# Optimization experiments

Hardware: AMD Instinct MI355X
Metric: run time of the kernel (lower is better)

The kernel has to match this reference:

```python
import jax, jax.numpy as jnp
import numpy as np
from jax import lax

EPS = 1e-5

def _sign(x):
    # sign with sign(0)=+1, as used in XNOR-style binarization
    return jnp.where(x >= 0, 1.0, -1.0).astype(x.dtype)

def binarize(x):
    # straight-through estimator: forward = sign(x), backward = identity
    return x + lax.stop_gradient(_sign(x) - x)

def batchnorm(x, p):
    # p: [4, C] rows = (gamma, beta, running_mean, running_var); eval-mode BN
    g, b, m, v = p[0], p[1], p[2], p[3]
    shape = (1, -1) + (1,) * (x.ndim - 2)
    inv = g / jnp.sqrt(v + EPS)
    return (x - m.reshape(shape)) * inv.reshape(shape) + b.reshape(shape)

def conv2d(x, w):
    return lax.conv_general_dilated(x, w, window_strides=(1, 1), padding='VALID',
                                    dimension_numbers=('NCHW', 'OIHW', 'NCHW'))

def maxpool2(x):
    return lax.reduce_window(x, -jnp.inf, lax.max, (1, 1, 2, 2), (1, 1, 2, 2), 'VALID')

def hardtanh(x):
    return jnp.clip(x, -1.0, 1.0)


def setup_inputs() -> dict:
    key = jax.random.key(0)
    ks = jax.random.split(key, 16)
    B = 16384
    x = jax.random.normal(ks[0], (B, 3, 22, 22), jnp.float32)
    w1 = jax.random.normal(ks[1], (32, 3, 3, 3), jnp.float32) * 0.1
    w2 = jax.random.normal(ks[2], (32, 32, 3, 3), jnp.float32) * 0.1
    w3 = jax.random.normal(ks[3], (64, 32, 3, 3), jnp.float32) * 0.1
    w_fc1 = jax.random.normal(ks[4], (128, 64), jnp.float32) * 0.1
    w_fc2 = jax.random.normal(ks[5], (2, 128), jnp.float32) * 0.1
    w_fc3 = jax.random.normal(ks[6], (4, 128), jnp.float32) * 0.1

    def make_bn(k, c):
        k1, k2, k3, k4 = jax.random.split(k, 4)
        gamma = jax.random.uniform(k1, (c,), jnp.float32, 0.5, 1.5)
        beta = jax.random.normal(k2, (c,), jnp.float32) * 0.1
        mean = jax.random.normal(k3, (c,), jnp.float32) * 0.1
        var = jax.random.uniform(k4, (c,), jnp.float32, 0.5, 1.5)
        return jnp.stack([gamma, beta, mean, var])  # [4, C]

    bn1 = make_bn(ks[7], 32)
    bn2 = make_bn(ks[8], 32)
    bn3 = make_bn(ks[9], 64)
    bn4 = make_bn(ks[10], 128)
    bn5 = make_bn(ks[11], 2)
    bn6 = make_bn(ks[12], 4)
    return {'x': x, 'w1': w1, 'w2': w2, 'w3': w3, 'w_fc1': w_fc1, 'w_fc2': w_fc2,
            'w_fc3': w_fc3, 'bn1': bn1, 'bn2': bn2, 'bn3': bn3, 'bn4': bn4,
            'bn5': bn5, 'bn6': bn6}


def reference(x, w1, w2, w3, w_fc1, w_fc2, w_fc3, bn1, bn2, bn3, bn4, bn5, bn6):
    # binary=True, binarize_input=True, bitwidth=input_bitwidth=1:
    # every BinarizeConv2d/BinarizeLinear binarizes both its input and weights.
    h = hardtanh(batchnorm(conv2d(binarize(x), binarize(w1)), bn1))   # [B,32,20,20]
    h = maxpool2(h)                                                    # [B,32,10,10]
    h = hardtanh(batchnorm(conv2d(binarize(h), binarize(w2)), bn2))   # [B,32,8,8]
    h = maxpool2(h)                                                    # [B,32,4,4]
    h = hardtanh(batchnorm(conv2d(binarize(h), binarize(w3)), bn3))   # [B,64,2,2]
    h = maxpool2(h)                                                    # [B,64,1,1]
    h = h.reshape(-1, 64)                                              # [B,64]
    h = hardtanh(batchnorm(binarize(h) @ binarize(w_fc1).T, bn4))      # [B,128]
    out1 = jax.nn.softmax(batchnorm(h @ w_fc2.T, bn5), axis=1)         # [B,2]
    out2 = batchnorm(h @ w_fc3.T, bn6)                                 # [B,4]
    return (out1, out2)
```

## Files before the change

### kernel.cpp

```cpp
#include <hip/hip_runtime.h>
#include <cstdint>
#include <cmath>

typedef int  v4i  __attribute__((ext_vector_type(4)));
typedef int  v16i __attribute__((ext_vector_type(16)));
typedef unsigned int u32x4 __attribute__((ext_vector_type(4)));

#define OFF_W1   0
#define OFF_T1   32
#define OFF_W3   384
#define OFF_T3   960
#define OFF_WFC1 1024
#define OFF_A4   1280
#define OFF_C4   1408
#define OFF_WF2  1536
#define OFF_WF3  1792
#define OFF_BN5  2304
#define OFF_BN6  2308
#define OFF_B2   2560
#define OFF_T2C  4864

__device__ __forceinline__ int thr_neg(double nterms, double g, double b, double m, double v) {
    double inv = g / sqrt(v + 1e-5);
    double t = m - b / inv;
    double thr = floor((nterms - t) * 0.5);
    if (thr < -2147000000.0) thr = -2147000000.0;
    if (thr >  2147000000.0) thr =  2147000000.0;
    return -((int)thr + 1);
}

__device__ __forceinline__ int thr_c_neg(double g, double b, double m, double v) {
    double inv = g / sqrt(v + 1e-5);
    double t = m - b / inv;
    double ct = ceil(t);
    if (ct < -2147000000.0) ct = -2147000000.0;
    if (ct >  2147000000.0) ct =  2147000000.0;
    return -(int)ct;
}

__global__ void k_prep(const float* __restrict__ w1, const float* __restrict__ w2,
                       const float* __restrict__ w3, const float* __restrict__ wfc1,
                       const float* __restrict__ wfc2, const float* __restrict__ wfc3,
                       const float* __restrict__ bn1, const float* __restrict__ bn2,
                       const float* __restrict__ bn3, const float* __restrict__ bn4,
                       const float* __restrict__ bn5, const float* __restrict__ bn6,
                       unsigned int* __restrict__ ws) {
    __shared__ float stage[9216];
    int t = threadIdx.x;
    int blk = blockIdx.x;
    float* wsf = (float*)ws;
    int*   wsi = (int*)ws;

    if (blk == 0) {
        for (int i = t; i < 864; i += 256) stage[i] = w1[i];
        __syncthreads();
        if (t < 32) {
            unsigned int bits = 0;
            for (int j = 0; j < 27; ++j) bits |= (stage[t*27+j] >= 0.f ? 1u : 0u) << j;
            ws[OFF_W1 + t] = bits;
            wsi[OFF_T1 + t]  = thr_neg(27.0, bn1[t], bn1[32+t], bn1[64+t], bn1[96+t]);
            wsi[OFF_T2C + t] = thr_c_neg(bn2[t], bn2[32+t], bn2[64+t], bn2[96+t]);
        }
        for (int i = t; i < 256; i += 256) wsf[OFF_WF2 + i] = wfc2[i];
        for (int i = t; i < 512; i += 256) wsf[OFF_WF3 + i] = wfc3[i];
        if (t < 2) {
            float g = bn5[t], b = bn5[2+t], m = bn5[4+t], v = bn5[6+t];
            float inv = g / sqrtf(v + 1e-5f);
            wsf[OFF_BN5 + t]     = inv;
            wsf[OFF_BN5 + 2 + t] = b - m * inv;
        }
        if (t >= 4 && t < 8) {
            int j = t - 4;
            float g = bn6[j], b = bn6[4+j], m = bn6[8+j], v = bn6[12+j];
            float inv = g / sqrtf(v + 1e-5f);
            wsf[OFF_BN6 + j]     = inv;
            wsf[OFF_BN6 + 4 + j] = b - m * inv;
        }
    } else if (blk == 1) {
        for (int i = t; i < 9216; i += 256) stage[i] = w2[i];
        __syncthreads();
        for (int idx = t; idx < 2304; idx += 256) {
            int s   = idx >> 8;
            int rem = idx & 255;
            int l   = rem >> 2;
            int reg = rem & 3;
            int och = l & 31;
            int icb = ((l >> 5) << 4) + (reg << 2);
            unsigned int wv = 0;
            #pragma unroll
            for (int j = 0; j < 4; ++j) {
                int ic = icb + j;
                unsigned int by = (stage[(och*32 + ic)*9 + s] >= 0.f) ? 0x01u : 0xFFu;
                wv |= by << (8*j);
            }
            ws[OFF_B2 + idx] = wv;
        }
    } else if (blk == 2 || blk == 3) {
        int base = (blk - 2) * 9216;
        for (int i = t; i < 9216; i += 256) stage[i] = w3[base + i];
        __syncthreads();
        for (int idx = t; idx < 288; idx += 256) {
            int o = idx / 9, k = idx - o*9;
            unsigned int bits = 0;
            for (int i = 0; i < 32; ++i)
                bits |= (stage[(o*32+i)*9 + k] >= 0.f ? 1u : 0u) << i;
            ws[OFF_W3 + base/32 + idx] = bits;
        }
    } else {
        for (int i = t; i < 8192; i += 256) stage[i] = wfc1[i];
        __syncthreads();
        if (t < 128) {
            unsigned int lo = 0, hi = 0;
            for (int j = 0; j < 32; ++j) lo |= (stage[t*64+j]    >= 0.f ? 1u : 0u) << j;
            for (int j = 0; j < 32; ++j) hi |= (stage[t*64+32+j] >= 0.f ? 1u : 0u) << j;
            ws[OFF_WFC1 + 2*t]     = lo;
            ws[OFF_WFC1 + 2*t + 1] = hi;
            float g = bn4[t], b = bn4[128+t], m = bn4[256+t], v = bn4[384+t];
            float inv = g / sqrtf(v + 1e-5f);
            wsf[OFF_A4 + t] = -2.f * inv;
            wsf[OFF_C4 + t] = (64.f - m) * inv + b;
        }
        if (t >= 128 && t < 192) {
            int j = t - 128;
            wsi[OFF_T3 + j] = thr_neg(288.0, bn3[j], bn3[64+j], bn3[128+j], bn3[192+j]);
        }
    }
}

#define WSTRIDE 900
__global__ __launch_bounds__(512, 6) void k_main(const float* __restrict__ x,
                                                 const unsigned int* __restrict__ ws,
                                                 float* __restrict__ out, int B) {
    __shared__ __align__(16) unsigned int s_u[8 * WSTRIDE + 2304];

    const int tid = threadIdx.x & 63;
    const int wid = threadIdx.x >> 6;
    const float* wsf = (const float*)ws;
    const int*   wsi = (const int*)ws;

    unsigned int* Blds  = s_u + 8 * WSTRIDE;
    unsigned int* bytes = s_u + wid * WSTRIDE;
    unsigned int* inrow = bytes;
    unsigned int* c1    = bytes + 66;
    unsigned int* pb1   = bytes + 800;

    for (int i = threadIdx.x; i < 576; i += 512)
        *(u32x4*)(Blds + i*4) = *(const u32x4*)(ws + OFF_B2 + i*4);
    __syncthreads();

    const int b = blockIdx.x * 8 + wid;
    if (b >= B) return;

    const int nthr2 = wsi[OFF_T2C + (tid & 31)];

    for (int r = tid; r < 66; r += 64) {
        int c = r / 22, y = r - c*22;
        const float2* p = (const float2*)(x + ((size_t)b*3 + c)*484 + (size_t)y*22);
        unsigned int w = 0;
        #pragma unroll
        for (int j = 10; j >= 0; --j) {
            float2 v = p[j];
            w = __builtin_amdgcn_alignbit(w, __float_as_uint(v.y), 31);
            w = __builtin_amdgcn_alignbit(w, __float_as_uint(v.x), 31);
        }
        inrow[r] = ~w;
    }
    __builtin_amdgcn_wave_barrier();

    for (int pos = tid; pos < 400; pos += 64) {
        int y = pos / 20, xx = pos - y*20;
        unsigned int g = 0;
        #pragma unroll
        for (int c = 0; c < 3; ++c)
            #pragma unroll
            for (int dy = 0; dy < 3; ++dy)
                g |= ((inrow[c*22 + y + dy] >> xx) & 7u) << (c*9 + dy*3);
        unsigned int word = 0;
        #pragma unroll
        for (int o = 31; o >= 0; --o) {
            unsigned int s = (unsigned int)(__popc(g ^ ws[OFF_W1 + o]) + wsi[OFF_T1 + o]);
            word = __builtin_amdgcn_alignbit(word, s, 31);
        }
        c1[pos] = word;
    }
    __builtin_amdgcn_wave_barrier();

    for (int p = tid; p < 100; p += 64) {
        int py = p / 10, px = p - py*10;
        int base = (2*py)*20 + 2*px;
        pb1[p] = c1[base] | c1[base+1] | c1[base+20] | c1[base+21];
    }
    __builtin_amdgcn_wave_barrier();

    #pragma unroll
    for (int i = 0; i < 4; ++i) {
        int c2 = tid + 64*i;
        if (c2 < 200) {
            int hi  = (c2 >= 100) ? 1 : 0;
            int pos = c2 - hi*100;
            unsigned int w = pb1[pos];
            int sh = hi << 4;
            u32x4 o;
            #pragma unroll
            for (int j = 0; j < 4; ++j) {
                unsigned int nib = (w >> (sh + 4*j)) & 0xFu;
                unsigned int sp  = (nib * 0x204081u) & 0x01010101u;
                o[j] = __builtin_amdgcn_perm(0u, 0x000001FFu, sp);
            }
            *(u32x4*)(bytes + c2*4) = o;
        }
    }
    __builtin_amdgcn_wave_barrier();

    unsigned int pb2w[16];
    {
        const int hi = tid >> 5;
        const int r  = tid & 31;
        #pragma unroll
        for (int tile = 0; tile < 2; ++tile) {
            int gq  = tile*8 + (r >> 2);
            int sub = r & 3;
            int y   = ((gq >> 2) << 1) + (sub >> 1);
            int x   = ((gq & 3) << 1) + (sub & 1);
            const v4i* __restrict__ Ab = (const v4i*)(bytes + (hi*100 + y*10 + x)*4);
            const v4i* __restrict__ Bb = (const v4i*)(Blds + tid*4);
            v16i acc;
            #pragma unroll
            for (int j = 0; j < 16; ++j) acc[j] = nthr2;
            __builtin_amdgcn_s_setprio(1);
            #pragma unroll
            for (int s = 0; s < 9; ++s) {
                int dy = s / 3, dx = s - dy*3;
                v4i a  = Ab[dy*10 + dx];
                v4i bf = Bb[s*64];
                acc = __builtin_amdgcn_mfma_i32_32x32x32_i8(a, bf, acc, 0, 0, 0);
            }
            __builtin_amdgcn_s_setprio(0);
            #pragma unroll
            for (int g = 0; g < 4; ++g) {
                int m0 = acc[4*g]   > acc[4*g+1] ? acc[4*g]   : acc[4*g+1];
                int m1 = acc[4*g+2] > acc[4*g+3] ? acc[4*g+2] : acc[4*g+3];
                int mx = m0 > m1 ? m0 : m1;
                unsigned long long bal = __ballot(mx >= 0);
                pb2w[tile*8 + 2*g]     = (unsigned int)bal;
                pb2w[tile*8 + 2*g + 1] = (unsigned int)(bal >> 32);
            }
        }
    }

    unsigned int w3r[9];
    #pragma unroll
    for (int k = 0; k < 9; ++k) w3r[k] = ws[OFF_W3 + tid*9 + k];
    const int negt3 = wsi[OFF_T3 + tid];

    unsigned long long b3 = 0;
    {
        unsigned int oracc = 0;
        #pragma unroll
        for (int py = 0; py < 2; ++py)
            #pragma unroll
            for (int px = 0; px < 2; ++px) {
                int s = negt3;
                #pragma unroll
                for (int dy = 0; dy < 3; ++dy)
                    #pragma unroll
                    for (int dx = 0; dx < 3; ++dx)
                        s += __popc(pb2w[(py+dy)*4 + px + dx] ^ w3r[dy*3+dx]);
                oracc |= (unsigned int)s;
            }
        b3 = __ballot((int)oracc < 0);
    }

    float h0, h1;
    {
        const unsigned long long* wfc1b = (const unsigned long long*)(ws + OFF_WFC1);
        int pc0 = __popcll(b3 ^ wfc1b[tid]);
        int pc1 = __popcll(b3 ^ wfc1b[tid + 64]);
        float p0 = fmaf((float)pc0, wsf[OFF_A4 + tid],      wsf[OFF_C4 + tid]);
        float p1 = fmaf((float)pc1, wsf[OFF_A4 + tid + 64], wsf[OFF_C4 + tid + 64]);
        h0 = fminf(1.f, fmaxf(-1.f, p0));
        h1 = fminf(1.f, fmaxf(-1.f, p1));
    }

    {
        float part[6];
        #pragma unroll
        for (int j = 0; j < 2; ++j)
            part[j] = h0 * wsf[OFF_WF2 + j*128 + tid] + h1 * wsf[OFF_WF2 + j*128 + 64 + tid];
        #pragma unroll
        for (int j = 0; j < 4; ++j)
            part[2+j] = h0 * wsf[OFF_WF3 + j*128 + tid] + h1 * wsf[OFF_WF3 + j*128 + 64 + tid];
        #pragma unroll
        for (int off = 32; off; off >>= 1) {
            #pragma unroll
            for (int j = 0; j < 6; ++j)
                part[j] += __shfl_xor(part[j], off);
        }
        if (tid < 6) {
            if (tid < 2) {
                float y0 = part[0]*wsf[OFF_BN5+0] + wsf[OFF_BN5+2];
                float y1 = part[1]*wsf[OFF_BN5+1] + wsf[OFF_BN5+3];
                float mx = fmaxf(y0, y1);
                float e0 = expf(y0 - mx), e1 = expf(y1 - mx);
                float r  = 1.f / (e0 + e1);
                out[(size_t)b*2 + tid] = (tid == 0 ? e0 : e1) * r;
            } else {
                int j = tid - 2;
                out[(size_t)B*2 + (size_t)b*4 + j] = part[2+j]*wsf[OFF_BN6+j] + wsf[OFF_BN6+4+j];
            }
        }
    }
}

extern "C" void kernel_launch(void* const* d_in, const int* in_sizes, int n_in,
                              void* d_out, int out_size, void* d_ws, size_t ws_size,
                              hipStream_t stream) {
    const float* x    = (const float*)d_in[0];
    const float* w1   = (const float*)d_in[1];
    const float* w2   = (const float*)d_in[2];
    const float* w3   = (const float*)d_in[3];
    const float* wfc1 = (const float*)d_in[4];
    const float* wfc2 = (const float*)d_in[5];
    const float* wfc3 = (const float*)d_in[6];
    const float* bn1  = (const float*)d_in[7];
    const float* bn2  = (const float*)d_in[8];
    const float* bn3  = (const float*)d_in[9];
    const float* bn4  = (const float*)d_in[10];
    const float* bn5  = (const float*)d_in[11];
    const float* bn6  = (const float*)d_in[12];
    unsigned int* ws  = (unsigned int*)d_ws;
    float* out        = (float*)d_out;
    int B = in_sizes[0] / 1452;

    k_prep<<<5, 256, 0, stream>>>(w1, w2, w3, wfc1, wfc2, wfc3,
                                  bn1, bn2, bn3, bn4, bn5, bn6, ws);
    k_main<<<(B + 7) / 8, 512, 0, stream>>>(x, ws, out, B);
}
```

Before: 182.4 us.

## Fuse conv1, maxpool and byte expansion per pooled output position

Each thread now computes the four conv1 outputs of a 2x2 pool window directly from the input bit rows. It takes the min of the four sign-test sums and writes the expanded byte operand for conv2, so the c1 and pb1 LDS buffers and two wave barriers are gone. This removes the LDS round trips and shrinks per-wave shared memory, which may help occupancy. It loads each weight and threshold once and reuses it across four popcounts. The cost is more registers and fewer active lanes, since 100 pooled positions now spread over 64 threads instead of 400 conv outputs.

```diff
diff --git a/kernel.cpp b/kernel.cpp
--- a/kernel.cpp
+++ b/kernel.cpp
@@ -127,7 +127,7 @@
     }
 }
 
-#define WSTRIDE 900
+#define WSTRIDE 868
 __global__ __launch_bounds__(512, 6) void k_main(const float* __restrict__ x,
                                                  const unsigned int* __restrict__ ws,
                                                  float* __restrict__ out, int B) {
@@ -139,10 +139,8 @@
     const int*   wsi = (const int*)ws;
 
     unsigned int* Blds  = s_u + 8 * WSTRIDE;
-    unsigned int* bytes = s_u + wid * WSTRIDE;
-    unsigned int* inrow = bytes;
-    unsigned int* c1    = bytes + 66;
-    unsigned int* pb1   = bytes + 800;
+    unsigned int* inrow = s_u + wid * WSTRIDE;
+    unsigned int* bytes = inrow + 68;
 
     for (int i = threadIdx.x; i < 576; i += 512)
         *(u32x4*)(Blds + i*4) = *(const u32x4*)(ws + OFF_B2 + i*4);
@@ -167,47 +165,56 @@
     }
     __builtin_amdgcn_wave_barrier();
 
-    for (int pos = tid; pos < 400; pos += 64) {
-        int y = pos / 20, xx = pos - y*20;
-        unsigned int g = 0;
-        #pragma unroll
-        for (int c = 0; c < 3; ++c)
-            #pragma unroll
-            for (int dy = 0; dy < 3; ++dy)
-                g |= ((inrow[c*22 + y + dy] >> xx) & 7u) << (c*9 + dy*3);
-        unsigned int word = 0;
-        #pragma unroll
-        for (int o = 31; o >= 0; --o) {
-            unsigned int s = (unsigned int)(__popc(g ^ ws[OFF_W1 + o]) + wsi[OFF_T1 + o]);
-            word = __builtin_amdgcn_alignbit(word, s, 31);
-        }
-        c1[pos] = word;
-    }
-    __builtin_amdgcn_wave_barrier();
-
-    for (int p = tid; p < 100; p += 64) {
-        int py = p / 10, px = p - py*10;
-        int base = (2*py)*20 + 2*px;
-        pb1[p] = c1[base] | c1[base+1] | c1[base+20] | c1[base+21];
-    }
-    __builtin_amdgcn_wave_barrier();
-
     #pragma unroll
-    for (int i = 0; i < 4; ++i) {
-        int c2 = tid + 64*i;
-        if (c2 < 200) {
-            int hi  = (c2 >= 100) ? 1 : 0;
-            int pos = c2 - hi*100;
-            unsigned int w = pb1[pos];
-            int sh = hi << 4;
-            u32x4 o;
-            #pragma unroll
-            for (int j = 0; j < 4; ++j) {
-                unsigned int nib = (w >> (sh + 4*j)) & 0xFu;
-                unsigned int sp  = (nib * 0x204081u) & 0x01010101u;
-                o[j] = __builtin_amdgcn_perm(0u, 0x000001FFu, sp);
-            }
-            *(u32x4*)(bytes + c2*4) = o;
+    for (int it = 0; it < 2; ++it) {
+        int q = tid + 64*it;
+        if (q < 100) {
+            int py = q / 10, px = q - py*10;
+            unsigned int g00 = 0, g01 = 0, g10 = 0, g11 = 0;
+            #pragma unroll
+            for (int c = 0; c < 3; ++c) {
+                unsigned int a0, a1, a2, a3, b0, b1, b2, b3;
+                {
+                    unsigned int w0 = (inrow[c*22 + 2*py + 0] >> (2*px)) & 15u;
+                    unsigned int w1 = (inrow[c*22 + 2*py + 1] >> (2*px)) & 15u;
+                    unsigned int w2 = (inrow[c*22 + 2*py + 2] >> (2*px)) & 15u;
+                    unsigned int w3 = (inrow[c*22 + 2*py + 3] >> (2*px)) & 15u;
+                    a0 = w0 & 7u; b0 = (w0 >> 1) & 7u;
+                    a1 = w1 & 7u; b1 = (w1 >> 1) & 7u;
+                    a2 = w2 & 7u; b2 = (w2 >> 1) & 7u;
+                    a3 = w3 & 7u; b3 = (w3 >> 1) & 7u;
+                }
+                int sh = c*9;
+                g00 |= (a0 | (a1 << 3) | (a2 << 6)) << sh;
+                g10 |= (a1 | (a2 << 3) | (a3 << 6)) << sh;
+                g01 |= (b0 | (b1 << 3) | (b2 << 6)) << sh;
+                g11 |= (b1 | (b2 << 3) | (b3 << 6)) << sh;
+            }
+            unsigned int pw = 0;
+            #pragma unroll
+            for (int o = 31; o >= 0; --o) {
+                unsigned int wv = ws[OFF_W1 + o];
+                int t0 = wsi[OFF_T1 + o];
+                int s0 = __popc(g00 ^ wv) + t0;
+                int s1 = __popc(g01 ^ wv) + t0;
+                int s2 = __popc(g10 ^ wv) + t0;
+                int s3 = __popc(g11 ^ wv) + t0;
+                int m0 = s0 < s1 ? s0 : s1;
+                int m1 = s2 < s3 ? s2 : s3;
+                int mn = m0 < m1 ? m0 : m1;
+                pw = __builtin_amdgcn_alignbit(pw, (unsigned int)mn, 31);
+            }
+            #pragma unroll
+            for (int hi = 0; hi < 2; ++hi) {
+                int sh = hi << 4;
+                u32x4 o4;
+                #pragma unroll
+                for (int j = 0; j < 4; ++j) {
+                    unsigned int nib = (pw >> (sh + 4*j)) & 0xFu;
+                    o4[j] = __builtin_amdgcn_perm(0u, 0x000001FFu, (nib * 0x204081u) & 0x01010101u);
+                }
+                *(u32x4*)(bytes + (hi*100 + q)*4) = o4;
+            }
         }
     }
     __builtin_amdgcn_wave_barrier();
```

After: 178.7 us. 1.02x faster.
